# Kernel tuning notes

Measured on AMD Instinct MI355X. Metric: run time of the kernel, lower is better.

## Reference

```python
import jax, jax.numpy as jnp
from jax import lax
import numpy as np

N_LAYERS = 2
HIDDEN = 1024
N_STOCKS = 1024
LB, UB = 0.0, 0.2
REBAL_ITERS = 32  # fixed upper bound; loop converges in 1-2 iters in practice


def setup_inputs() -> dict:
    key = jax.random.key(0)
    ks = jax.random.split(key, 20)
    B, T = 512, 128
    inp = {"x": jax.random.normal(ks[0], (B, T, N_STOCKS), dtype=jnp.float32)}
    k = 1
    for l in range(N_LAYERS):
        in_dim = N_STOCKS if l == 0 else HIDDEN
        s = 1.0 / np.sqrt(HIDDEN)
        inp[f"w_ih_{l}"] = jax.random.uniform(ks[k], (3 * HIDDEN, in_dim), minval=-s, maxval=s); k += 1
        inp[f"w_hh_{l}"] = jax.random.uniform(ks[k], (3 * HIDDEN, HIDDEN), minval=-s, maxval=s); k += 1
        inp[f"b_ih_{l}"] = jax.random.uniform(ks[k], (3 * HIDDEN,), minval=-s, maxval=s); k += 1
        inp[f"b_hh_{l}"] = jax.random.uniform(ks[k], (3 * HIDDEN,), minval=-s, maxval=s); k += 1
    s = 1.0 / np.sqrt(HIDDEN)
    inp["fc_w"] = jax.random.uniform(ks[k], (N_STOCKS, HIDDEN), minval=-s, maxval=s); k += 1
    inp["fc_b"] = jax.random.uniform(ks[k], (N_STOCKS,), minval=-s, maxval=s)
    return inp


def _gru_layer(x, w_ih, w_hh, b_ih, b_hh):
    # x: [B,T,D] -> hidden sequence [B,T,H]; PyTorch GRU cell math
    B, T, _ = x.shape
    H = w_hh.shape[1]
    x_proj = jnp.einsum('btd,gd->btg', x, w_ih) + b_ih  # [B,T,3H]

    def step(h, xp):
        hp = h @ w_hh.T + b_hh
        xr, xz, xn = jnp.split(xp, 3, axis=-1)
        hr, hz, hn = jnp.split(hp, 3, axis=-1)
        r = jax.nn.sigmoid(xr + hr)
        z = jax.nn.sigmoid(xz + hz)
        n = jnp.tanh(xn + r * hn)
        h_new = (1.0 - z) * n + z * h
        return h_new, h_new

    h0 = jnp.zeros((B, H), x.dtype)
    _, hs = lax.scan(step, h0, jnp.swapaxes(x_proj, 0, 1))  # [T,B,H]
    return jnp.swapaxes(hs, 0, 1)


def _rebalance(w, lb, ub, n_iters=REBAL_ITERS):
    # Batched version of the iterative capped-simplex redistribution loop.
    old = w
    wc = jnp.clip(w, lb, ub)
    done = jnp.zeros((w.shape[0],), dtype=bool)

    def body(state, _):
        old, wc, done = state
        leftover = jnp.sum(old - wc, axis=-1, keepdims=True)            # [B,1]
        mask = wc != ub                                                  # nominees
        num = jnp.sum(mask, axis=-1)                                     # [B]
        nom_sum = jnp.sum(jnp.where(mask, wc, 0.0), axis=-1, keepdims=True)
        gift = leftover * wc / jnp.where(nom_sum == 0.0, 1.0, nom_sum)
        wc_new = jnp.where(mask, wc + gift, wc)
        no_nom = num == 0
        over = jnp.any(wc_new > ub, axis=-1)
        new_done = done | no_nom | (~over)
        wc_next = jnp.where(no_nom[:, None], wc,
                            jnp.where(over[:, None], jnp.clip(wc_new, lb, ub), wc_new))
        old_next = jnp.where(no_nom[:, None], old, wc_new)
        wc_out = jnp.where(done[:, None], wc, wc_next)
        old_out = jnp.where(done[:, None], old, old_next)
        return (old_out, wc_out, new_done), None

    (_, wc, _), _ = lax.scan(body, (old, wc, done), None, length=n_iters)
    return wc


def reference(x, w_ih_0, w_hh_0, b_ih_0, b_hh_0, w_ih_1, w_hh_1, b_ih_1, b_hh_1, fc_w, fc_b):
    h = _gru_layer(x, w_ih_0, w_hh_0, b_ih_0, b_hh_0)
    h = _gru_layer(h, w_ih_1, w_hh_1, b_ih_1, b_hh_1)
    h_t = h[:, -1, :]                                   # last time step [B,H]
    logit = h_t @ fc_w.T + fc_b                         # dropout is identity in eval
    logit = jax.nn.silu(logit)
    probs = jax.nn.softmax(logit, axis=-1)
    return _rebalance(probs, LB, UB)
```

## Files before the change

kernel.cpp:

```cpp
#include <hip/hip_runtime.h>
#include <hip/hip_bf16.h>
#include <stdint.h>

#define BB 512
#define TT 128
#define DD 1024
#define HH 1024
#define G3 3072
#define TC 32
#define NCH (TT/TC)
#define NRING 33

typedef __bf16 bft;
typedef __bf16 bf16x8 __attribute__((ext_vector_type(8)));
typedef float f32x4 __attribute__((ext_vector_type(4)));

__device__ __forceinline__ void gl_lds16(const bft* g, void* lds_base_uniform) {
  __builtin_amdgcn_global_load_lds(
      (const __attribute__((address_space(1))) void*)g,
      (__attribute__((address_space(3))) void*)lds_base_uniform,
      16, 0, 0);
}

__device__ __forceinline__ void st_wt_bf16(bft* p, float v) {
  bft h = (bft)v;
  union { bft h; unsigned short u; } cv; cv.h = h;
  unsigned int uv = cv.u;
  asm volatile("global_store_short %0, %1, off sc0 sc1" :: "v"(p), "v"(uv) : "memory");
}
__device__ __forceinline__ void st_wt_f32(float* p, float v) {
  asm volatile("global_store_dword %0, %1, off sc0 sc1" :: "v"(p), "v"(v) : "memory");
}
__device__ __forceinline__ void st_wt_u32(int* p, int v) {
  asm volatile("global_store_dword %0, %1, off sc0 sc1" :: "v"(p), "v"(v) : "memory");
}
__device__ __forceinline__ int ld_co_u32(const int* p) {
  int v;
  asm volatile("global_load_dword %0, %1, off sc0 sc1\n\ts_waitcnt vmcnt(0)"
               : "=v"(v) : "v"(p) : "memory");
  return v;
}

__device__ __forceinline__ float fexp2(float x) {
  float r; asm("v_exp_f32 %0, %1" : "=v"(r) : "v"(x)); return r;
}
__device__ __forceinline__ float frcp(float x) {
  float r; asm("v_rcp_f32 %0, %1" : "=v"(r) : "v"(x)); return r;
}
#define LOG2E 1.44269504f

__global__ void k_cvt(const float* __restrict__ in, bft* __restrict__ out, long n) {
  long i = ((long)blockIdx.x * blockDim.x + threadIdx.x) * 8;
  long stride = (long)gridDim.x * blockDim.x * 8;
  for (; i < n; i += stride) {
    float4 a = *(const float4*)(in + i);
    float4 b = *(const float4*)(in + i + 4);
    bf16x8 r;
    r[0] = (bft)a.x; r[1] = (bft)a.y; r[2] = (bft)a.z; r[3] = (bft)a.w;
    r[4] = (bft)b.x; r[5] = (bft)b.y; r[6] = (bft)b.z; r[7] = (bft)b.w;
    *(bf16x8*)(out + i) = r;
  }
}

template<int AMODE, int EPI>
__launch_bounds__(256)
__global__ void k_gemm(const void* __restrict__ Ap, long lda,
                       const bft* __restrict__ W, long ldw,
                       const float* __restrict__ bias,
                       void* __restrict__ Cout, long ldc,
                       int t0, int K) {
  __shared__ unsigned char sm[32768];
  const int tid  = threadIdx.x;
  const int lane = tid & 63;
  const int wid  = tid >> 6;
  const int m0 = blockIdx.y * 128;
  const int n0 = blockIdx.x * 128;
  const int wm = wid >> 1, wn = wid & 1;

  f32x4 acc[4][4] = {};

  for (int k0 = 0; k0 < K; k0 += 64) {
    if (AMODE == 1) {
      const float* Af = (const float*)Ap;
#pragma unroll
      for (int s = 0; s < 4; ++s) {
        int seg = wid * 4 + s;
        int row = seg * 8 + (lane >> 3);
        int mr = m0 + row;
        long grow = (long)(mr >> 5) * TT + t0 + (mr & 31);
        const float* src = Af + grow * lda + k0 + (lane & 7) * 8;
        float4 a  = *(const float4*)src;
        float4 b2 = *(const float4*)(src + 4);
        bf16x8 r;
        r[0] = (bft)a.x;  r[1] = (bft)a.y;  r[2] = (bft)a.z;  r[3] = (bft)a.w;
        r[4] = (bft)b2.x; r[5] = (bft)b2.y; r[6] = (bft)b2.z; r[7] = (bft)b2.w;
        *(bf16x8*)(sm + seg * 1024 + (lane >> 3) * 128 +
                   (((lane & 7) * 16) ^ ((row & 7) << 4))) = r;
      }
    } else {
      const bft* Ab = (const bft*)Ap;
#pragma unroll
      for (int s = 0; s < 4; ++s) {
        int seg = wid * 4 + s;
        int row = seg * 8 + (lane >> 3);
        int cbs = ((lane & 7) * 16) ^ ((row & 7) << 4);
        int mr = m0 + row;
        long grow;
        if (AMODE == 0) grow = mr;
        else { int sl = t0 + (mr & 31); if (sl >= NRING) sl -= NRING;
               grow = (long)sl * BB + (mr >> 5); }
        gl_lds16(Ab + grow * lda + k0 + (cbs >> 1), sm + seg * 1024);
      }
    }
#pragma unroll
    for (int s = 0; s < 4; ++s) {
      int seg = wid * 4 + s;
      int row = seg * 8 + (lane >> 3);
      int cbs = ((lane & 7) * 16) ^ ((row & 7) << 4);
      gl_lds16(W + (long)(n0 + row) * ldw + k0 + (cbs >> 1), sm + 16384 + seg * 1024);
    }
    __syncthreads();
#pragma unroll
    for (int ks = 0; ks < 2; ++ks) {
      int kb = ks * 64 + (lane >> 4) * 16;
      bf16x8 aF[4], bF[4];
#pragma unroll
      for (int mi = 0; mi < 4; ++mi) {
        int row = wm * 64 + mi * 16 + (lane & 15);
        aF[mi] = *(const bf16x8*)(sm + row * 128 + (kb ^ ((row & 7) << 4)));
      }
#pragma unroll
      for (int ni = 0; ni < 4; ++ni) {
        int row = wn * 64 + ni * 16 + (lane & 15);
        bF[ni] = *(const bf16x8*)(sm + 16384 + row * 128 + (kb ^ ((row & 7) << 4)));
      }
#pragma unroll
      for (int mi = 0; mi < 4; ++mi)
#pragma unroll
        for (int ni = 0; ni < 4; ++ni)
          acc[mi][ni] = __builtin_amdgcn_mfma_f32_16x16x32_bf16(aF[mi], bF[ni], acc[mi][ni], 0, 0, 0);
    }
    __syncthreads();
  }

#pragma unroll
  for (int mi = 0; mi < 4; ++mi)
#pragma unroll
    for (int ni = 0; ni < 4; ++ni) {
      int col = n0 + wn * 64 + ni * 16 + (lane & 15);
      float bv = bias[col];
#pragma unroll
      for (int r = 0; r < 4; ++r) {
        long row = m0 + wm * 64 + mi * 16 + (lane >> 4) * 4 + r;
        float v = acc[mi][ni][r] + bv;
        if (EPI == 0) {
          ((bft*)Cout)[row * ldc + col] = (bft)v;
        } else {
          ((float*)Cout)[row * ldc + col] = v / (1.f + expf(-v));
        }
      }
    }
}

__launch_bounds__(256, 1)
__global__ void k_persist(const bft* __restrict__ whh, const float* __restrict__ bhh,
                          const bft* __restrict__ xp,
                          bft* __restrict__ ring,
                          float* __restrict__ hfc, int* __restrict__ flags,
                          int t0s, int first, int pbase) {
  __shared__ unsigned char sm[98304];
  unsigned char* smW = sm;
  unsigned char* smA = sm + 32768;

  const int tid  = threadIdx.x;
  const int lane = tid & 63;
  const int wid  = tid >> 6;
  const int bid  = blockIdx.x;
  const int xcd = bid & 7, loc = bid >> 3;
  const int mt = xcd >> 1;
  const int nt = (xcd & 1) * 32 + loc;
  const int j0 = nt * 16;
  const int m0 = mt * 128;
  const int j  = j0 + (lane & 15);
  int* gflags = flags + mt * 64;

#pragma unroll
  for (int s8 = 0; s8 < 8; ++s8) {
    int s = wid * 8 + s8;
    int row = s >> 1;
    int half = s & 1;
    int hb = half * 1024 + lane * 16;
    int sb = hb ^ ((row & 7) << 4);
    long grow = (long)(2 * 1024 + j0 + row);
    gl_lds16(whh + grow * 1024 + (sb >> 1), smW + s * 1024);
  }

  bf16x8 wrz[2][16][2];
#pragma unroll
  for (int g = 0; g < 2; ++g) {
    const bft* wbase = whh + (((long)g * 1024 + j) << 10) + ((lane >> 4) * 8);
#pragma unroll
    for (int k = 0; k < 16; ++k)
#pragma unroll
      for (int ks = 0; ks < 2; ++ks) {
        bf16x8 wl = *(const bf16x8*)(wbase + k * 64 + ks * 32);
        asm("" : "=a"(wrz[g][k][ks]) : "0"(wl));
      }
  }
  asm volatile("s_waitcnt vmcnt(0)" ::: "memory");
  __builtin_amdgcn_s_barrier();

  const float br = bhh[j], bz = bhh[1024 + j], bn = bhh[2048 + j];

  auto stageA = [&](const bft* base, int k0, int bufsel) {
    unsigned char* dst = smA + bufsel * 16384;
#pragma unroll
    for (int si = 0; si < 4; ++si) {
      int seg = wid * 4 + si;
      int row = seg * 8 + (lane >> 3);
      int cb = ((lane & 7) * 16) ^ ((row & 7) << 4);
      gl_lds16(base + (long)(m0 + row) * DD + k0 + (cb >> 1), dst + seg * 1024);
    }
  };

  float xg[3][2][4];
  float hp[2][4];

  auto prefXG = [&](int s) {
#pragma unroll
    for (int mi = 0; mi < 2; ++mi)
#pragma unroll
      for (int r = 0; r < 4; ++r) {
        long b = m0 + wid * 32 + mi * 16 + (lane >> 4) * 4 + r;
        long xrow = (b * TC + s) * (long)G3 + j;
        xg[0][mi][r] = (float)xp[xrow];
        xg[1][mi][r] = (float)xp[xrow + 1024];
        xg[2][mi][r] = (float)xp[xrow + 2048];
      }
  };

  prefXG(0);
  if (first) {
#pragma unroll
    for (int mi = 0; mi < 2; ++mi)
#pragma unroll
      for (int r = 0; r < 4; ++r) hp[mi][r] = 0.f;
  } else {
#pragma unroll
    for (int mi = 0; mi < 2; ++mi)
#pragma unroll
      for (int r = 0; r < 4; ++r) {
        long b = m0 + wid * 32 + mi * 16 + (lane >> 4) * 4 + r;
        hp[mi][r] = hfc[b * HH + j];
      }
  }
  __builtin_amdgcn_sched_barrier(0);

  for (int s = 0; s < TC; ++s) {
    if (s) {
      int target = pbase + s;
      if (tid < 64) {
        const int* fp = gflags + tid;
        while (ld_co_u32(fp) < target) __builtin_amdgcn_s_sleep(1);
      }
      __syncthreads();
    }

    int sl = t0s + s; if (sl >= NRING) sl -= NRING;
    int psl = sl ? sl - 1 : NRING - 1;

    f32x4 acc[3][2] = {};
    if (!(first && s == 0)) {
      const bft* Ab = ring + (long)psl * (BB * (long)DD);
      stageA(Ab, 0, 0);
      stageA(Ab, 64, 1);
      stageA(Ab, 128, 2);
#pragma unroll
      for (int k = 0; k < 16; ++k) {
        __builtin_amdgcn_sched_barrier(0);
        if (k < 13) stageA(Ab, (k + 3) * 64, (k + 3) & 3);
        if (k < 13)       asm volatile("s_waitcnt vmcnt(12)" ::: "memory");
        else if (k == 13) asm volatile("s_waitcnt vmcnt(8)" ::: "memory");
        else if (k == 14) asm volatile("s_waitcnt vmcnt(4)" ::: "memory");
        else              asm volatile("s_waitcnt vmcnt(0)" ::: "memory");
        __builtin_amdgcn_sched_barrier(0);
        const unsigned char* Abuf = smA + (k & 3) * 16384;
#pragma unroll
        for (int ks = 0; ks < 2; ++ks) {
          int kb = ks * 64 + (lane >> 4) * 16;
          bf16x8 aF[2];
#pragma unroll
          for (int mi = 0; mi < 2; ++mi) {
            int row = wid * 32 + mi * 16 + (lane & 15);
            aF[mi] = *(const bf16x8*)(Abuf + row * 128 + (kb ^ ((row & 7) << 4)));
          }
          int wrow = lane & 15;
          bf16x8 bFn = *(const bf16x8*)(smW + wrow * 2048 +
                                        ((k * 128 + kb) ^ ((wrow & 7) << 4)));
#pragma unroll
          for (int mi = 0; mi < 2; ++mi) {
            acc[0][mi] = __builtin_amdgcn_mfma_f32_16x16x32_bf16(aF[mi], wrz[0][k][ks], acc[0][mi], 0, 0, 0);
            acc[1][mi] = __builtin_amdgcn_mfma_f32_16x16x32_bf16(aF[mi], wrz[1][k][ks], acc[1][mi], 0, 0, 0);
            acc[2][mi] = __builtin_amdgcn_mfma_f32_16x16x32_bf16(aF[mi], bFn,           acc[2][mi], 0, 0, 0);
          }
        }
      }
    }

    bft* outp = ring + (long)sl * (BB * (long)DD);
#pragma unroll
    for (int mi = 0; mi < 2; ++mi)
#pragma unroll
      for (int r = 0; r < 4; ++r) {
        long b = m0 + wid * 32 + mi * 16 + (lane >> 4) * 4 + r;
        float hr = acc[0][mi][r] + br;
        float hz = acc[1][mi][r] + bz;
        float hn = acc[2][mi][r] + bn;
        float rg = frcp(1.f + fexp2(-LOG2E * (xg[0][mi][r] + hr)));
        float zg = frcp(1.f + fexp2(-LOG2E * (xg[1][mi][r] + hz)));
        float e2 = fexp2(2.f * LOG2E * (xg[2][mi][r] + rg * hn));
        float ng = 1.f - 2.f * frcp(e2 + 1.f);
        float hv = (1.f - zg) * ng + zg * hp[mi][r];
        hp[mi][r] = hv;
        st_wt_bf16(outp + b * DD + j, hv);
        if (s == TC - 1) st_wt_f32(hfc + b * HH + j, hv);
      }

    __syncthreads();
    if (s < TC - 1) {
      if (tid == 0) st_wt_u32(gflags + nt, pbase + s + 1);
      prefXG(s + 1);
      __builtin_amdgcn_sched_barrier(0);
    }
  }
}

__device__ __forceinline__ float blk_sum(float v, float* red, int tid) {
#pragma unroll
  for (int o = 32; o; o >>= 1) v += __shfl_xor(v, o);
  if ((tid & 63) == 0) red[tid >> 6] = v;
  __syncthreads();
  v = red[0] + red[1] + red[2] + red[3];
  __syncthreads();
  return v;
}
__device__ __forceinline__ float blk_max(float v, float* red, int tid) {
#pragma unroll
  for (int o = 32; o; o >>= 1) v = fmaxf(v, __shfl_xor(v, o));
  if ((tid & 63) == 0) red[tid >> 6] = v;
  __syncthreads();
  v = fmaxf(fmaxf(red[0], red[1]), fmaxf(red[2], red[3]));
  __syncthreads();
  return v;
}

__launch_bounds__(256)
__global__ void k_smrebal(const float* __restrict__ logits, float* __restrict__ out) {
  __shared__ float red[4];
  const int tid = threadIdx.x;
  const long row = blockIdx.x;
  const float ub = 0.2f, lb = 0.0f;
  float4 lv = *(const float4*)(logits + row * 1024 + tid * 4);

  float m = fmaxf(fmaxf(lv.x, lv.y), fmaxf(lv.z, lv.w));
  m = blk_max(m, red, tid);
  float e[4] = {expf(lv.x - m), expf(lv.y - m), expf(lv.z - m), expf(lv.w - m)};
  float S = blk_sum(e[0] + e[1] + e[2] + e[3], red, tid);

  float old_[4], wc[4];
#pragma unroll
  for (int k = 0; k < 4; ++k) {
    float p = e[k] / S;
    old_[k] = p;
    wc[k] = fminf(fmaxf(p, lb), ub);
  }
  bool done = false;
  for (int it = 0; it < 32 && !done; ++it) {
    float d3 = 0.f, cnt = 0.f, nsum = 0.f;
#pragma unroll
    for (int k = 0; k < 4; ++k) {
      d3 += old_[k] - wc[k];
      bool mk = (wc[k] != ub);
      cnt += mk ? 1.f : 0.f;
      nsum += mk ? wc[k] : 0.f;
    }
    float leftover = blk_sum(d3, red, tid);
    float num = blk_sum(cnt, red, tid);
    float nom_sum = blk_sum(nsum, red, tid);
    float denom = (nom_sum == 0.f) ? 1.f : nom_sum;
    float wcn[4], mx = -1e30f;
#pragma unroll
    for (int k = 0; k < 4; ++k) {
      bool mk = (wc[k] != ub);
      wcn[k] = mk ? wc[k] + leftover * wc[k] / denom : wc[k];
      mx = fmaxf(mx, wcn[k]);
    }
    float gmx = blk_max(mx, red, tid);
    bool no_nom = (num == 0.f);
    bool over = (gmx > ub);
#pragma unroll
    for (int k = 0; k < 4; ++k) {
      float nxt = no_nom ? wc[k] : (over ? fminf(fmaxf(wcn[k], lb), ub) : wcn[k]);
      float oldn = no_nom ? old_[k] : wcn[k];
      wc[k] = nxt;
      old_[k] = oldn;
    }
    done = no_nom || !over;
  }
#pragma unroll
  for (int k = 0; k < 4; ++k) out[row * 1024 + tid * 4 + k] = wc[k];
}

extern "C" void kernel_launch(void* const* d_in, const int* in_sizes, int n_in,
                              void* d_out, int out_size, void* d_ws, size_t ws_size,
                              hipStream_t stream) {
  const float* x      = (const float*)d_in[0];
  const float* wih[2] = {(const float*)d_in[1], (const float*)d_in[5]};
  const float* whh[2] = {(const float*)d_in[2], (const float*)d_in[6]};
  const float* bih[2] = {(const float*)d_in[3], (const float*)d_in[7]};
  const float* bhh[2] = {(const float*)d_in[4], (const float*)d_in[8]};
  const float* fcw    = (const float*)d_in[9];
  const float* fcb    = (const float*)d_in[10];
  float* outp = (float*)d_out;

  unsigned char* ws = (unsigned char*)d_ws;
  size_t off = 0;
  auto alloc = [&](size_t bytes) -> void* {
    void* p = ws + off;
    off += (bytes + 255) & ~(size_t)255;
    return p;
  };
  bft* wihb0   = (bft*)alloc((size_t)G3 * DD * 2);
  bft* whhb0   = (bft*)alloc((size_t)G3 * HH * 2);
  bft* wihb1   = (bft*)alloc((size_t)G3 * HH * 2);
  bft* whhb1   = (bft*)alloc((size_t)G3 * HH * 2);
  bft* fcwb    = (bft*)alloc((size_t)1024 * 1024 * 2);
  bft* xp      = (bft*)alloc((size_t)BB * TC * G3 * 2);
  bft* ring0   = (bft*)alloc((size_t)NRING * BB * DD * 2);
  bft* ring1   = (bft*)alloc((size_t)NRING * BB * DD * 2);
  float* hfc0  = (float*)alloc((size_t)BB * HH * 4);
  float* hfc1  = (float*)alloc((size_t)BB * HH * 4);
  int* flags   = (int*)alloc(1024);
  float* logits= (float*)alloc((size_t)BB * 1024 * 4);
  if (off > ws_size) return;

  hipMemsetAsync(flags, 0, 1024, stream);

  k_cvt<<<dim3(1536), dim3(256), 0, stream>>>(wih[0], wihb0, (long)G3 * DD);
  k_cvt<<<dim3(1536), dim3(256), 0, stream>>>(whh[0], whhb0, (long)G3 * HH);
  k_cvt<<<dim3(1536), dim3(256), 0, stream>>>(wih[1], wihb1, (long)G3 * HH);
  k_cvt<<<dim3(1536), dim3(256), 0, stream>>>(whh[1], whhb1, (long)G3 * HH);
  k_cvt<<<dim3(512),  dim3(256), 0, stream>>>(fcw, fcwb, (long)1024 * 1024);

  for (int c = 0; c < NCH; ++c) {
    int t0 = c * TC;
    int t0s = t0 % NRING;
    int first = (c == 0) ? 1 : 0;
    k_gemm<1, 0><<<dim3(G3 / 128, (BB * TC) / 128), 256, 0, stream>>>(
        x, DD, wihb0, DD, bih[0], xp, G3, t0, DD);
    k_persist<<<dim3(256), dim3(256), 0, stream>>>(
        whhb0, bhh[0], xp, ring0, hfc0, flags, t0s, first, (2 * c) * TC);
    k_gemm<2, 0><<<dim3(G3 / 128, (BB * TC) / 128), 256, 0, stream>>>(
        ring0, DD, wihb1, DD, bih[1], xp, G3, t0s, DD);
    k_persist<<<dim3(256), dim3(256), 0, stream>>>(
        whhb1, bhh[1], xp, ring1, hfc1, flags, t0s, first, (2 * c + 1) * TC);
  }
  const bft* hfin = ring1 + (size_t)((TT - 1) % NRING) * BB * DD;
  k_gemm<0, 1><<<dim3(1024 / 128, BB / 128), 256, 0, stream>>>(
      hfin, DD, fcwb, HH, fcb, logits, 1024, 0, HH);
  k_smrebal<<<dim3(BB), 256, 0, stream>>>(logits, outp);
}
```

Measured before the change: 2.701 ms.

## Replace chunked ring-buffer pipeline with full-sequence projection and single persistent scan

Removes the four-way time chunking (32-step chunks with a 33-slot ring buffer and saved f32 hidden state) so that each layer runs one input-projection GEMM over all 128 timesteps, followed by a single persistent recurrent kernel over the whole sequence. Full hidden-state sequences and the full x projection buffer are now kept in the workspace. The big GEMMs get an XCD-aware tile swizzle for L2 locality. This cuts the kernel launch count and the per-chunk persistent-kernel startup (weight staging) from four launches per layer to one, at the cost of a much larger workspace and less chance for GEMM/scan overlap across chunks.

```diff
diff --git a/kernel.cpp b/kernel.cpp
--- a/kernel.cpp
+++ b/kernel.cpp
@@ -7,9 +7,6 @@
 #define DD 1024
 #define HH 1024
 #define G3 3072
-#define TC 32
-#define NCH (TT/TC)
-#define NRING 33
 
 typedef __bf16 bft;
 typedef __bf16 bf16x8 __attribute__((ext_vector_type(8)));
@@ -27,9 +24,6 @@
   union { bft h; unsigned short u; } cv; cv.h = h;
   unsigned int uv = cv.u;
   asm volatile("global_store_short %0, %1, off sc0 sc1" :: "v"(p), "v"(uv) : "memory");
-}
-__device__ __forceinline__ void st_wt_f32(float* p, float v) {
-  asm volatile("global_store_dword %0, %1, off sc0 sc1" :: "v"(p), "v"(v) : "memory");
 }
 __device__ __forceinline__ void st_wt_u32(int* p, int v) {
   asm volatile("global_store_dword %0, %1, off sc0 sc1" :: "v"(p), "v"(v) : "memory");
@@ -62,19 +56,29 @@
   }
 }
 
-template<int AMODE, int EPI>
+template<int AMODE, int EPI, int SWZ>
 __launch_bounds__(256)
 __global__ void k_gemm(const void* __restrict__ Ap, long lda,
                        const bft* __restrict__ W, long ldw,
                        const float* __restrict__ bias,
                        void* __restrict__ Cout, long ldc,
-                       int t0, int K) {
+                       int K) {
   __shared__ unsigned char sm[32768];
   const int tid  = threadIdx.x;
   const int lane = tid & 63;
   const int wid  = tid >> 6;
-  const int m0 = blockIdx.y * 128;
-  const int n0 = blockIdx.x * 128;
+  int m_t, n_t;
+  if (SWZ) {
+    int lin = blockIdx.x + blockIdx.y * gridDim.x;
+    int xcd = lin & 7, idx = lin >> 3;
+    int xm = xcd >> 1, xn = xcd & 1;
+    int bi = idx >> 4, wi = idx & 15;
+    int nb = bi / 32, mb = bi - nb * 32;
+    m_t = xm * 128 + mb * 4 + (wi & 3);
+    n_t = xn * 12 + nb * 4 + (wi >> 2);
+  } else { m_t = blockIdx.y; n_t = blockIdx.x; }
+  const int m0 = m_t * 128;
+  const int n0 = n_t * 128;
   const int wm = wid >> 1, wn = wid & 1;
 
   f32x4 acc[4][4] = {};
@@ -86,8 +90,7 @@
       for (int s = 0; s < 4; ++s) {
         int seg = wid * 4 + s;
         int row = seg * 8 + (lane >> 3);
-        int mr = m0 + row;
-        long grow = (long)(mr >> 5) * TT + t0 + (mr & 31);
+        long grow = (long)(m0 + row);
         const float* src = Af + grow * lda + k0 + (lane & 7) * 8;
         float4 a  = *(const float4*)src;
         float4 b2 = *(const float4*)(src + 4);
@@ -107,8 +110,7 @@
         int mr = m0 + row;
         long grow;
         if (AMODE == 0) grow = mr;
-        else { int sl = t0 + (mr & 31); if (sl >= NRING) sl -= NRING;
-               grow = (long)sl * BB + (mr >> 5); }
+        else            grow = (long)(mr & (TT - 1)) * BB + (mr >> 7);
         gl_lds16(Ab + grow * lda + k0 + (cbs >> 1), sm + seg * 1024);
       }
     }
@@ -165,9 +167,8 @@
 __launch_bounds__(256, 1)
 __global__ void k_persist(const bft* __restrict__ whh, const float* __restrict__ bhh,
                           const bft* __restrict__ xp,
-                          bft* __restrict__ ring,
-                          float* __restrict__ hfc, int* __restrict__ flags,
-                          int t0s, int first, int pbase) {
+                          bft* __restrict__ hseq,
+                          int* __restrict__ flags, int pbase) {
   __shared__ unsigned char sm[98304];
   unsigned char* smW = sm;
   unsigned char* smA = sm + 32768;
@@ -232,7 +233,7 @@
 #pragma unroll
       for (int r = 0; r < 4; ++r) {
         long b = m0 + wid * 32 + mi * 16 + (lane >> 4) * 4 + r;
-        long xrow = (b * TC + s) * (long)G3 + j;
+        long xrow = (b * (long)TT + s) * (long)G3 + j;
         xg[0][mi][r] = (float)xp[xrow];
         xg[1][mi][r] = (float)xp[xrow + 1024];
         xg[2][mi][r] = (float)xp[xrow + 2048];
@@ -240,23 +241,14 @@
   };
 
   prefXG(0);
-  if (first) {
-#pragma unroll
-    for (int mi = 0; mi < 2; ++mi)
-#pragma unroll
-      for (int r = 0; r < 4; ++r) hp[mi][r] = 0.f;
-  } else {
-#pragma unroll
-    for (int mi = 0; mi < 2; ++mi)
-#pragma unroll
-      for (int r = 0; r < 4; ++r) {
-        long b = m0 + wid * 32 + mi * 16 + (lane >> 4) * 4 + r;
-        hp[mi][r] = hfc[b * HH + j];
-      }
-  }
+#pragma unroll
+  for (int mi = 0; mi < 2; ++mi)
+#pragma unroll
+    for (int r = 0; r < 4; ++r) hp[mi][r] = 0.f;
   __builtin_amdgcn_sched_barrier(0);
 
-  for (int s = 0; s < TC; ++s) {
+#pragma unroll 1
+  for (int s = 0; s < TT; ++s) {
     if (s) {
       int target = pbase + s;
       if (tid < 64) {
@@ -266,12 +258,9 @@
       __syncthreads();
     }
 
-    int sl = t0s + s; if (sl >= NRING) sl -= NRING;
-    int psl = sl ? sl - 1 : NRING - 1;
-
     f32x4 acc[3][2] = {};
-    if (!(first && s == 0)) {
-      const bft* Ab = ring + (long)psl * (BB * (long)DD);
+    if (s) {
+      const bft* Ab = hseq + (long)(s - 1) * (BB * (long)DD);
       stageA(Ab, 0, 0);
       stageA(Ab, 64, 1);
       stageA(Ab, 128, 2);
@@ -307,7 +296,7 @@
       }
     }
 
-    bft* outp = ring + (long)sl * (BB * (long)DD);
+    bft* outp = hseq + (long)s * (BB * (long)DD);
 #pragma unroll
     for (int mi = 0; mi < 2; ++mi)
 #pragma unroll
@@ -323,11 +312,10 @@
         float hv = (1.f - zg) * ng + zg * hp[mi][r];
         hp[mi][r] = hv;
         st_wt_bf16(outp + b * DD + j, hv);
-        if (s == TC - 1) st_wt_f32(hfc + b * HH + j, hv);
       }
 
     __syncthreads();
-    if (s < TC - 1) {
+    if (s < TT - 1) {
       if (tid == 0) st_wt_u32(gflags + nt, pbase + s + 1);
       prefXG(s + 1);
       __builtin_amdgcn_sched_barrier(0);
@@ -435,11 +423,9 @@
   bft* wihb1   = (bft*)alloc((size_t)G3 * HH * 2);
   bft* whhb1   = (bft*)alloc((size_t)G3 * HH * 2);
   bft* fcwb    = (bft*)alloc((size_t)1024 * 1024 * 2);
-  bft* xp      = (bft*)alloc((size_t)BB * TC * G3 * 2);
-  bft* ring0   = (bft*)alloc((size_t)NRING * BB * DD * 2);
-  bft* ring1   = (bft*)alloc((size_t)NRING * BB * DD * 2);
-  float* hfc0  = (float*)alloc((size_t)BB * HH * 4);
-  float* hfc1  = (float*)alloc((size_t)BB * HH * 4);
+  bft* xp      = (bft*)alloc((size_t)BB * TT * G3 * 2);
+  bft* hseq0   = (bft*)alloc((size_t)TT * BB * DD * 2);
+  bft* hseq1   = (bft*)alloc((size_t)TT * BB * DD * 2);
   int* flags   = (int*)alloc(1024);
   float* logits= (float*)alloc((size_t)BB * 1024 * 4);
   if (off > ws_size) return;
@@ -452,21 +438,17 @@
   k_cvt<<<dim3(1536), dim3(256), 0, stream>>>(whh[1], whhb1, (long)G3 * HH);
   k_cvt<<<dim3(512),  dim3(256), 0, stream>>>(fcw, fcwb, (long)1024 * 1024);
 
-  for (int c = 0; c < NCH; ++c) {
-    int t0 = c * TC;
-    int t0s = t0 % NRING;
-    int first = (c == 0) ? 1 : 0;
-    k_gemm<1, 0><<<dim3(G3 / 128, (BB * TC) / 128), 256, 0, stream>>>(
-        x, DD, wihb0, DD, bih[0], xp, G3, t0, DD);
-    k_persist<<<dim3(256), dim3(256), 0, stream>>>(
-        whhb0, bhh[0], xp, ring0, hfc0, flags, t0s, first, (2 * c) * TC);
-    k_gemm<2, 0><<<dim3(G3 / 128, (BB * TC) / 128), 256, 0, stream>>>(
-        ring0, DD, wihb1, DD, bih[1], xp, G3, t0s, DD);
-    k_persist<<<dim3(256), dim3(256), 0, stream>>>(
-        whhb1, bhh[1], xp, ring1, hfc1, flags, t0s, first, (2 * c + 1) * TC);
-  }
-  const bft* hfin = ring1 + (size_t)((TT - 1) % NRING) * BB * DD;
-  k_gemm<0, 1><<<dim3(1024 / 128, BB / 128), 256, 0, stream>>>(
-      hfin, DD, fcwb, HH, fcb, logits, 1024, 0, HH);
+  k_gemm<1, 0, 1><<<dim3(24, 512), 256, 0, stream>>>(
+      x, DD, wihb0, DD, bih[0], xp, G3, DD);
+  k_persist<<<dim3(256), dim3(256), 0, stream>>>(
+      whhb0, bhh[0], xp, hseq0, flags, 0);
+  k_gemm<2, 0, 1><<<dim3(24, 512), 256, 0, stream>>>(
+      hseq0, DD, wihb1, DD, bih[1], xp, G3, DD);
+  k_persist<<<dim3(256), dim3(256), 0, stream>>>(
+      whhb1, bhh[1], xp, hseq1, flags, TT);
+
+  const bft* hfin = hseq1 + (size_t)(TT - 1) * BB * DD;
+  k_gemm<0, 1, 0><<<dim3(1024 / 128, BB / 128), 256, 0, stream>>>(
+      hfin, DD, fcwb, HH, fcb, logits, 1024, HH);
   k_smrebal<<<dim3(BB), 256, 0, stream>>>(logits, outp);
 }
```

Measured after the change: 2.790 ms. 1.03x slower.
